# Performance work log

Measured on AMD Instinct MI355X. Metric: run time of the kernel, lower is better.

The kernel has to match this reference:

```python
import jax, jax.numpy as jnp
import numpy as np

N_EXPERTS = 8
TOP_K = 2
D_MODEL = 1024
N_TOKENS = 8192


def setup_inputs() -> dict:
    key = jax.random.key(0)
    k1, k2, k3, k4, k5 = jax.random.split(key, 5)
    x = jax.random.normal(k1, (N_TOKENS, D_MODEL), dtype=jnp.float32)
    # router Linear(num_experts): weight [d, E], bias [E]
    Wr = jax.random.normal(k2, (D_MODEL, N_EXPERTS), dtype=jnp.float32) / np.sqrt(D_MODEL)
    br = jnp.zeros((N_EXPERTS,), dtype=jnp.float32)
    # per-expert Linear(d_model): stacked weights [E, d, d], biases [E, d]
    W = jax.random.normal(k3, (N_EXPERTS, D_MODEL, D_MODEL), dtype=jnp.float32) / np.sqrt(D_MODEL)
    b = jnp.zeros((N_EXPERTS, D_MODEL), dtype=jnp.float32)
    return {"x": x, "Wr": Wr, "br": br, "W": W, "b": b}


def reference(x, Wr, br, W, b):
    # --- route ---
    logits = x @ Wr + br                                  # [N, E]
    top_k_vals, top_k_idxs = jax.lax.top_k(logits, TOP_K)  # [N, k]
    top_k_gates = jax.nn.softmax(top_k_vals, axis=-1)      # [N, k]
    # --- experts (dense form of gather-dispatch; same math as routed compute) ---
    y_all = jnp.einsum('nd,edh->neh', x, W) + b            # [N, E, d]
    # --- gather routed expert outputs per slot ---
    y_k = jnp.take_along_axis(y_all, top_k_idxs[:, :, None], axis=1)  # [N, k, d]
    # --- weighted scatter-combine (reduce) ---
    out = jnp.sum(top_k_gates[:, :, None] * y_k, axis=1)   # [N, d]
    return out
```

## Files before the change

### kernel.cpp

```cpp
#include <hip/hip_runtime.h>
#include <hip/hip_bf16.h>


#define NTOK 8192
#define DM   1024
#define NEXP 8
#define CAP  8192
#define MAXT 136

#define RBLK 1024
#define WBLK 512

typedef __attribute__((ext_vector_type(8))) short bf16x8;
typedef __attribute__((ext_vector_type(4))) float f32x4;

__device__ __forceinline__ unsigned short f2bf(float f) {
  unsigned u = __float_as_uint(f);
  unsigned r = (u + 0x7fffu + ((u >> 16) & 1u)) >> 16;
  return (unsigned short)r;
}
__device__ __forceinline__ float bf2f(unsigned short s) {
  return __uint_as_float(((unsigned)s) << 16);
}

__device__ __forceinline__ void gl_lds16(const void* g, void* l) {
  __builtin_amdgcn_global_load_lds(
      (const __attribute__((address_space(1))) unsigned int*)g,
      (__attribute__((address_space(3))) unsigned int*)l, 16, 0, 0);
}

__global__ __launch_bounds__(256) void router_kernel(
    const float* __restrict__ x, const float* __restrict__ Wr,
    const float* __restrict__ br, unsigned short* __restrict__ xbf,
    int4* __restrict__ topk, int* __restrict__ counts,
    int* __restrict__ tok, int2* __restrict__ pos,
    int* __restrict__ done, int* __restrict__ desc,
    int* __restrict__ ntiles, int* __restrict__ offset) {
  __shared__ int lcnt[NEXP];
  __shared__ int4 ltop[8];
  __shared__ int2 lrank[8];
  const int tid = threadIdx.x;
  const int rb = blockIdx.x;
  const int wave = tid >> 6, lane = tid & 63;
  const int tb = rb * 8 + wave * 2;
  if (tid < NEXP) lcnt[tid] = 0;

  const int l4 = lane * 4;

  float v[2][16];
#pragma unroll
  for (int tt = 0; tt < 2; tt++) {
#pragma unroll
    for (int i = 0; i < 4; i++) {
      float4 f = *(const float4*)(x + (size_t)(tb + tt) * DM + i * 256 + l4);
      v[tt][i * 4 + 0] = f.x; v[tt][i * 4 + 1] = f.y;
      v[tt][i * 4 + 2] = f.z; v[tt][i * 4 + 3] = f.w;
    }
  }
#pragma unroll
  for (int tt = 0; tt < 2; tt++) {
#pragma unroll
    for (int i = 0; i < 4; i++) {
      uint2 pk;
      pk.x = (unsigned)f2bf(v[tt][i * 4 + 0]) |
             ((unsigned)f2bf(v[tt][i * 4 + 1]) << 16);
      pk.y = (unsigned)f2bf(v[tt][i * 4 + 2]) |
             ((unsigned)f2bf(v[tt][i * 4 + 3]) << 16);
      *(uint2*)(xbf + (size_t)(tb + tt) * DM + i * 256 + l4) = pk;
    }
  }
  float p[2][8] = {};
#pragma unroll
  for (int i = 0; i < 4; i++) {
#pragma unroll
    for (int j = 0; j < 4; j++) {
      const float* wrow = Wr + (size_t)(i * 256 + l4 + j) * NEXP;
      float4 wl = *(const float4*)(wrow);
      float4 wh = *(const float4*)(wrow + 4);
#pragma unroll
      for (int tt = 0; tt < 2; tt++) {
        float xv = v[tt][i * 4 + j];
        p[tt][0] += xv * wl.x; p[tt][1] += xv * wl.y;
        p[tt][2] += xv * wl.z; p[tt][3] += xv * wl.w;
        p[tt][4] += xv * wh.x; p[tt][5] += xv * wh.y;
        p[tt][6] += xv * wh.z; p[tt][7] += xv * wh.w;
      }
    }
  }
#pragma unroll
  for (int off = 32; off >= 1; off >>= 1) {
#pragma unroll
    for (int tt = 0; tt < 2; tt++)
#pragma unroll
      for (int e = 0; e < 8; e++)
        p[tt][e] += __shfl_xor(p[tt][e], off, 64);
  }
  if (lane == 0) {
#pragma unroll
    for (int tt = 0; tt < 2; tt++) {
      float lg[8];
#pragma unroll
      for (int e = 0; e < 8; e++) lg[e] = p[tt][e] + br[e];
      float v0 = lg[0]; int i0 = 0;
#pragma unroll
      for (int e = 1; e < 8; e++) if (lg[e] > v0) { v0 = lg[e]; i0 = e; }
      float v1 = -3.4e38f; int i1 = 0;
#pragma unroll
      for (int e = 0; e < 8; e++)
        if (e != i0 && lg[e] > v1) { v1 = lg[e]; i1 = e; }
      float ee = __expf(v1 - v0);
      float g0 = 1.0f / (1.0f + ee);
      float g1 = ee / (1.0f + ee);
      int4 rec;
      rec.x = i0; rec.y = i1;
      rec.z = __float_as_int(g0); rec.w = __float_as_int(g1);
      ltop[wave * 2 + tt] = rec;
      topk[tb + tt] = rec;
    }
  }
  __syncthreads();

  if (tid < 8) {
    int4 r = ltop[tid];
    int s0 = atomicAdd(&lcnt[r.x], 1);
    int s1 = atomicAdd(&lcnt[r.y], 1);
    int2 rk; rk.x = s0; rk.y = s1;
    lrank[tid] = rk;
  }
  __syncthreads();
  if (tid < NEXP) lcnt[tid] = atomicAdd(&counts[tid], lcnt[tid]);
  __syncthreads();
  if (tid < 8) {
    int4 r = ltop[tid];
    int2 rk = lrank[tid];
    int p0 = lcnt[r.x] + rk.x;
    int p1 = lcnt[r.y] + rk.y;
    int t = rb * 8 + tid;
    tok[r.x * CAP + p0] = t;
    tok[r.y * CAP + p1] = t;
    int2 pr; pr.x = p0; pr.y = p1;
    pos[t] = pr;
  }
  __syncthreads();

  if (tid == 0) {
    __threadfence();
    if (atomicAdd(done, 1) == RBLK - 1) {
      __threadfence();
      int cnt[NEXP];
#pragma unroll
      for (int e = 0; e < NEXP; e++) cnt[e] = atomicAdd(&counts[e], 0);
      int idx = 0, off = 0;
#pragma unroll
      for (int e = 0; e < NEXP; e++) {
        offset[e] = off;
        off += cnt[e];
        int nm = (cnt[e] + 127) >> 7;
        for (int i = 0; i < nm; i++) desc[idx++] = (e << 16) | i;
      }
      *ntiles = idx;
    }
  }
}

__global__ __launch_bounds__(256) void wcast_kernel(
    const float* __restrict__ W, unsigned short* __restrict__ Wt) {
  __shared__ __align__(16) unsigned int smem[8192];
  const int tid = threadIdx.x;
  const int tb = blockIdx.x;
  const int e = tb >> 6;
  const int rem = tb & 63;
  const int D0 = (rem >> 3) * 128;
  const int H0 = (rem & 7) * 128;

  const int dp = tid >> 5;
  const int c  = tid & 31;
  const float* Wsrc = W + (size_t)e * DM * DM + (size_t)D0 * DM + H0 + c * 4;
#pragma unroll 4
  for (int i = 0; i < 8; i++) {
    const int dc = dp + 8 * i;
    const int d = dc * 2;
    float4 a = *(const float4*)(Wsrc + (size_t)d * DM);
    float4 b = *(const float4*)(Wsrc + (size_t)(d + 1) * DM);
    unsigned pk[4];
    pk[0] = (unsigned)f2bf(a.x) | ((unsigned)f2bf(b.x) << 16);
    pk[1] = (unsigned)f2bf(a.y) | ((unsigned)f2bf(b.y) << 16);
    pk[2] = (unsigned)f2bf(a.z) | ((unsigned)f2bf(b.z) << 16);
    pk[3] = (unsigned)f2bf(a.w) | ((unsigned)f2bf(b.w) << 16);
#pragma unroll
    for (int j = 0; j < 4; j++) {
      const int h = c * 4 + j;
      const int pg = ((dc >> 2) ^ (h >> 2)) & 15;
      smem[h * 64 + pg * 4 + (dc & 3)] = pk[j];
    }
  }
  __syncthreads();

  const int hh = tid >> 4;
  const int g  = tid & 15;
  unsigned short* Wdst = Wt + (size_t)e * DM * DM + (size_t)H0 * DM + D0;
#pragma unroll 4
  for (int o = 0; o < 8; o++) {
    const int h = hh + 16 * o;
    const int pg = (g ^ (h >> 2)) & 15;
    uint4 v = *(const uint4*)(smem + h * 64 + pg * 4);
    *(uint4*)(Wdst + (size_t)h * DM + g * 8) = v;
  }
}

__global__ __launch_bounds__(256) void moe_gemm_kernel(
    const unsigned short* __restrict__ xbf, const unsigned short* __restrict__ wt,
    const int* __restrict__ counts, const int* __restrict__ offset,
    const int* __restrict__ tok, const int* __restrict__ desc,
    const int* __restrict__ ntiles, unsigned short* __restrict__ ybuf) {
  const int slot = blockIdx.y;
  if (slot >= *ntiles) return;
  const int dsc = desc[slot];
  const int e = dsc >> 16;
  const int m0 = (dsc & 0xffff) * 128;
  const int cnt = counts[e];
  const int n0 = blockIdx.x * 128;

  __shared__ __align__(16) unsigned short sA0[128 * 32];
  __shared__ __align__(16) unsigned short sB0[128 * 32];
  __shared__ __align__(16) unsigned short sA1[128 * 32];
  __shared__ __align__(16) unsigned short sB1[128 * 32];
  __shared__ int sTok[128];

  const int tid = threadIdx.x, wave = tid >> 6, lane = tid & 63;

  if (tid < 128) {
    int sr = m0 + tid;
    int cl = (sr < cnt) ? sr : (cnt - 1);
    sTok[tid] = tok[e * CAP + cl];
  }
  __syncthreads();

  const int rA1 = wave * 16 + (lane >> 2);
  const int rA2 = rA1 + 64;
  const int cch = lane & 3;
  const int cg1 = (cch ^ ((rA1 >> 1) & 3)) * 8;
  const int cg2 = (cch ^ ((rA2 >> 1) & 3)) * 8;
  const unsigned short* pA1 = xbf + (size_t)sTok[rA1] * DM + cg1;
  const unsigned short* pA2 = xbf + (size_t)sTok[rA2] * DM + cg2;
  const unsigned short* wte = wt + (size_t)e * DM * DM;
  const unsigned short* pB1 = wte + (size_t)(n0 + rA1) * DM + cg1;
  const unsigned short* pB2 = wte + (size_t)(n0 + rA2) * DM + cg2;
  const int lo1 = wave * 512, lo2 = (wave + 4) * 512;

  const int q = lane >> 4, ml = lane & 15;
  const int wm = (wave >> 1) * 64, wn = (wave & 1) * 64;
  int offA[4], offB[4];
#pragma unroll
  for (int i = 0; i < 4; i++) {
    int row = wm + i * 16 + ml;
    offA[i] = row * 32 + (q ^ ((row >> 1) & 3)) * 8;
    int rowb = wn + i * 16 + ml;
    offB[i] = rowb * 32 + (q ^ ((rowb >> 1) & 3)) * 8;
  }

  f32x4 acc[4][4] = {};

  for (int k0 = 0; k0 < DM; k0 += 64) {
    gl_lds16(pA1 + k0, sA0 + lo1);
    gl_lds16(pA2 + k0, sA0 + lo2);
    gl_lds16(pB1 + k0, sB0 + lo1);
    gl_lds16(pB2 + k0, sB0 + lo2);
    gl_lds16(pA1 + k0 + 32, sA1 + lo1);
    gl_lds16(pA2 + k0 + 32, sA1 + lo2);
    gl_lds16(pB1 + k0 + 32, sB1 + lo1);
    gl_lds16(pB2 + k0 + 32, sB1 + lo2);
    __syncthreads();
    bf16x8 af0[4], bf0[4], af1[4], bf1[4];
#pragma unroll
    for (int i = 0; i < 4; i++) {
      af0[i] = *(const bf16x8*)(sA0 + offA[i]);
      bf0[i] = *(const bf16x8*)(sB0 + offB[i]);
      af1[i] = *(const bf16x8*)(sA1 + offA[i]);
      bf1[i] = *(const bf16x8*)(sB1 + offB[i]);
    }
#pragma unroll
    for (int mt = 0; mt < 4; mt++)
#pragma unroll
      for (int nt = 0; nt < 4; nt++)
        acc[mt][nt] = __builtin_amdgcn_mfma_f32_16x16x32_bf16(
            af0[mt], bf0[nt], acc[mt][nt], 0, 0, 0);
#pragma unroll
    for (int mt = 0; mt < 4; mt++)
#pragma unroll
      for (int nt = 0; nt < 4; nt++)
        acc[mt][nt] = __builtin_amdgcn_mfma_f32_16x16x32_bf16(
            af1[mt], bf1[nt], acc[mt][nt], 0, 0, 0);
    __syncthreads();
  }

  const int yb = offset[e] + m0;
#pragma unroll
  for (int mt = 0; mt < 4; mt++) {
    int rbase = wm + mt * 16 + q * 4;
#pragma unroll
    for (int r = 0; r < 4; r++) {
      int row = rbase + r;
      if (m0 + row >= cnt) continue;
      unsigned short* yrow = ybuf + (size_t)(yb + row) * DM + n0;
#pragma unroll
      for (int nt = 0; nt < 4; nt++) {
        yrow[wn + nt * 16 + ml] = f2bf(acc[mt][nt][r]);
      }
    }
  }
}

__global__ __launch_bounds__(256) void combine_kernel(
    const unsigned short* __restrict__ ybuf, const int4* __restrict__ topk,
    const int2* __restrict__ pos, const int* __restrict__ offset,
    const float* __restrict__ bias, float* __restrict__ out) {
  const int c = threadIdx.x * 4;
  const int t0 = blockIdx.x * 4;
#pragma unroll
  for (int i = 0; i < 4; i++) {
    const int t = t0 + i;
    int4 r = topk[t];
    int2 p = pos[t];
    float g0 = __int_as_float(r.z), g1 = __int_as_float(r.w);
    int s0 = offset[r.x] + p.x;
    int s1 = offset[r.y] + p.y;
    ushort4 ya = *(const ushort4*)(ybuf + (size_t)s0 * DM + c);
    ushort4 yb = *(const ushort4*)(ybuf + (size_t)s1 * DM + c);
    float4 b0 = *(const float4*)(bias + (size_t)r.x * DM + c);
    float4 b1 = *(const float4*)(bias + (size_t)r.y * DM + c);
    float4 o;
    o.x = g0 * (bf2f(ya.x) + b0.x) + g1 * (bf2f(yb.x) + b1.x);
    o.y = g0 * (bf2f(ya.y) + b0.y) + g1 * (bf2f(yb.y) + b1.y);
    o.z = g0 * (bf2f(ya.z) + b0.z) + g1 * (bf2f(yb.z) + b1.z);
    o.w = g0 * (bf2f(ya.w) + b0.w) + g1 * (bf2f(yb.w) + b1.w);
    *(float4*)(out + (size_t)t * DM + c) = o;
  }
}

extern "C" void kernel_launch(void* const* d_in, const int* in_sizes, int n_in,
                              void* d_out, int out_size, void* d_ws, size_t ws_size,
                              hipStream_t stream) {
  const float* x  = (const float*)d_in[0];
  const float* Wr = (const float*)d_in[1];
  const float* br = (const float*)d_in[2];
  const float* W  = (const float*)d_in[3];
  const float* b  = (const float*)d_in[4];
  float* out = (float*)d_out;

  char* ws = (char*)d_ws;
  unsigned short* xbf  = (unsigned short*)ws;
  unsigned short* wt   = (unsigned short*)(ws + (16u << 20));
  unsigned short* ybuf = (unsigned short*)(ws + (32u << 20));
  char* ctrl = ws + (64u << 20);
  int*   counts = (int*)ctrl;
  int*   ntiles = (int*)(ctrl + 64);
  int*   done   = (int*)(ctrl + 96);
  int*   offset = (int*)(ctrl + 128);
  int*   desc   = (int*)(ctrl + 256);
  int*   tok    = (int*)(ctrl + 4096);
  int2*  pos    = (int2*)(ctrl + 4096 + (256u << 10));
  int4*  topk   = (int4*)(ctrl + 4096 + (320u << 10));

  hipMemsetAsync(ctrl, 0, 128, stream);

  router_kernel<<<RBLK, 256, 0, stream>>>(
      x, Wr, br, xbf, topk, counts, tok, pos, done, desc, ntiles, offset);
  wcast_kernel<<<WBLK, 256, 0, stream>>>(W, wt);
  moe_gemm_kernel<<<dim3(8, MAXT), 256, 0, stream>>>(
      xbf, wt, counts, offset, tok, desc, ntiles, ybuf);
  combine_kernel<<<NTOK / 4, 256, 0, stream>>>(ybuf, topk, pos, offset, b, out);
}
```

Before: 225.7 us.

## Double-buffer MoE GEMM LDS tiles and remap block indices for weight reuse

Adds a second LDS buffer so the global-to-LDS loads for the next K step are issued before the MFMA work on the current step, overlapping memory latency with compute. It also remaps the linear block index so eight consecutive blocks cover different token tiles that share the same N column slice, which is meant to improve L2 reuse of expert weight columns. LDS use doubles to 64KB per block, which may reduce occupancy.

```diff
diff --git a/kernel.cpp b/kernel.cpp
--- a/kernel.cpp
+++ b/kernel.cpp
@@ -213,18 +213,17 @@
     const int* __restrict__ counts, const int* __restrict__ offset,
     const int* __restrict__ tok, const int* __restrict__ desc,
     const int* __restrict__ ntiles, unsigned short* __restrict__ ybuf) {
-  const int slot = blockIdx.y;
+  const int L = blockIdx.y * 8 + blockIdx.x;
+  const int slot = (L & 7) | ((L >> 6) << 3);
+  const int n0 = ((L >> 3) & 7) * 128;
   if (slot >= *ntiles) return;
   const int dsc = desc[slot];
   const int e = dsc >> 16;
   const int m0 = (dsc & 0xffff) * 128;
   const int cnt = counts[e];
-  const int n0 = blockIdx.x * 128;
-
-  __shared__ __align__(16) unsigned short sA0[128 * 32];
-  __shared__ __align__(16) unsigned short sB0[128 * 32];
-  __shared__ __align__(16) unsigned short sA1[128 * 32];
-  __shared__ __align__(16) unsigned short sB1[128 * 32];
+
+  __shared__ __align__(16) unsigned short sA[2][2][128 * 32];
+  __shared__ __align__(16) unsigned short sB[2][2][128 * 32];
   __shared__ int sTok[128];
 
   const int tid = threadIdx.x, wave = tid >> 6, lane = tid & 63;
@@ -259,25 +258,40 @@
     offB[i] = rowb * 32 + (q ^ ((rowb >> 1) & 3)) * 8;
   }
 
+#define STAGE(b, kk)                                  \
+  do {                                                \
+    gl_lds16(pA1 + (kk),      &sA[b][0][lo1]);        \
+    gl_lds16(pA2 + (kk),      &sA[b][0][lo2]);        \
+    gl_lds16(pB1 + (kk),      &sB[b][0][lo1]);        \
+    gl_lds16(pB2 + (kk),      &sB[b][0][lo2]);        \
+    gl_lds16(pA1 + (kk) + 32, &sA[b][1][lo1]);        \
+    gl_lds16(pA2 + (kk) + 32, &sA[b][1][lo2]);        \
+    gl_lds16(pB1 + (kk) + 32, &sB[b][1][lo1]);        \
+    gl_lds16(pB2 + (kk) + 32, &sB[b][1][lo2]);        \
+  } while (0)
+
   f32x4 acc[4][4] = {};
 
+  STAGE(0, 0);
+  asm volatile("s_waitcnt vmcnt(0)" ::: "memory");
+  __builtin_amdgcn_s_barrier();
+
+  int cur = 0;
   for (int k0 = 0; k0 < DM; k0 += 64) {
-    gl_lds16(pA1 + k0, sA0 + lo1);
-    gl_lds16(pA2 + k0, sA0 + lo2);
-    gl_lds16(pB1 + k0, sB0 + lo1);
-    gl_lds16(pB2 + k0, sB0 + lo2);
-    gl_lds16(pA1 + k0 + 32, sA1 + lo1);
-    gl_lds16(pA2 + k0 + 32, sA1 + lo2);
-    gl_lds16(pB1 + k0 + 32, sB1 + lo1);
-    gl_lds16(pB2 + k0 + 32, sB1 + lo2);
-    __syncthreads();
+    if (k0 + 64 < DM) STAGE(cur ^ 1, k0 + 64);
+    __builtin_amdgcn_sched_barrier(0);
+
+    const unsigned short* a0 = sA[cur][0];
+    const unsigned short* b0 = sB[cur][0];
+    const unsigned short* a1 = sA[cur][1];
+    const unsigned short* b1 = sB[cur][1];
     bf16x8 af0[4], bf0[4], af1[4], bf1[4];
 #pragma unroll
     for (int i = 0; i < 4; i++) {
-      af0[i] = *(const bf16x8*)(sA0 + offA[i]);
-      bf0[i] = *(const bf16x8*)(sB0 + offB[i]);
-      af1[i] = *(const bf16x8*)(sA1 + offA[i]);
-      bf1[i] = *(const bf16x8*)(sB1 + offB[i]);
+      af0[i] = *(const bf16x8*)(a0 + offA[i]);
+      bf0[i] = *(const bf16x8*)(b0 + offB[i]);
+      af1[i] = *(const bf16x8*)(a1 + offA[i]);
+      bf1[i] = *(const bf16x8*)(b1 + offB[i]);
     }
 #pragma unroll
     for (int mt = 0; mt < 4; mt++)
@@ -291,8 +305,12 @@
       for (int nt = 0; nt < 4; nt++)
         acc[mt][nt] = __builtin_amdgcn_mfma_f32_16x16x32_bf16(
             af1[mt], bf1[nt], acc[mt][nt], 0, 0, 0);
-    __syncthreads();
-  }
+
+    asm volatile("s_waitcnt vmcnt(0)" ::: "memory");
+    __builtin_amdgcn_s_barrier();
+    cur ^= 1;
+  }
+#undef STAGE
 
   const int yb = offset[e] + m0;
 #pragma unroll
```

Measured after the change: 231.5 us. 1.03x slower.

## Stage router weights in LDS, split tile building, remap GEMM block order

Applied to the files above, without the earlier changes.

The router kernel now copies Wr into padded shared memory and reads x with lane-strided scalar loads, replacing the per-lane float4 global loads of Wr. The last-block atomic counter that built the tile descriptors moves into a separate single-thread kernel, which removes the threadfence and done atomic. The GEMM block index is remapped so that 8 consecutive blocks cover 8 M-tiles for the same N column, aiming for better L2 reuse of expert weights. In exchange there is one extra kernel launch, a 36 KB LDS load in every router block, and narrower (scalar) global accesses.

```diff
diff --git a/kernel.cpp b/kernel.cpp
--- a/kernel.cpp
+++ b/kernel.cpp
@@ -33,58 +33,43 @@
     const float* __restrict__ x, const float* __restrict__ Wr,
     const float* __restrict__ br, unsigned short* __restrict__ xbf,
     int4* __restrict__ topk, int* __restrict__ counts,
-    int* __restrict__ tok, int2* __restrict__ pos,
-    int* __restrict__ done, int* __restrict__ desc,
-    int* __restrict__ ntiles, int* __restrict__ offset) {
-  __shared__ int lcnt[NEXP];
+    int* __restrict__ tok, int2* __restrict__ pos) {
+  __shared__ float sWr[1024 * 9];
+  __shared__ int  lcnt[NEXP];
   __shared__ int4 ltop[8];
   __shared__ int2 lrank[8];
   const int tid = threadIdx.x;
-  const int rb = blockIdx.x;
   const int wave = tid >> 6, lane = tid & 63;
-  const int tb = rb * 8 + wave * 2;
+  const int tb = blockIdx.x * 8 + wave * 2;
   if (tid < NEXP) lcnt[tid] = 0;
 
-  const int l4 = lane * 4;
-
-  float v[2][16];
+#pragma unroll
+  for (int it = 0; it < 4; it++) {
+    const int row = it * 256 + tid;
+    float4 w0 = *(const float4*)(Wr + (size_t)row * 8);
+    float4 w1 = *(const float4*)(Wr + (size_t)row * 8 + 4);
+    float* dst = &sWr[row * 9];
+    dst[0] = w0.x; dst[1] = w0.y; dst[2] = w0.z; dst[3] = w0.w;
+    dst[4] = w1.x; dst[5] = w1.y; dst[6] = w1.z; dst[7] = w1.w;
+  }
+  __syncthreads();
+
+  float p[2][8] = {{0}};
 #pragma unroll
   for (int tt = 0; tt < 2; tt++) {
-#pragma unroll
-    for (int i = 0; i < 4; i++) {
-      float4 f = *(const float4*)(x + (size_t)(tb + tt) * DM + i * 256 + l4);
-      v[tt][i * 4 + 0] = f.x; v[tt][i * 4 + 1] = f.y;
-      v[tt][i * 4 + 2] = f.z; v[tt][i * 4 + 3] = f.w;
-    }
-  }
-#pragma unroll
-  for (int tt = 0; tt < 2; tt++) {
-#pragma unroll
-    for (int i = 0; i < 4; i++) {
-      uint2 pk;
-      pk.x = (unsigned)f2bf(v[tt][i * 4 + 0]) |
-             ((unsigned)f2bf(v[tt][i * 4 + 1]) << 16);
-      pk.y = (unsigned)f2bf(v[tt][i * 4 + 2]) |
-             ((unsigned)f2bf(v[tt][i * 4 + 3]) << 16);
-      *(uint2*)(xbf + (size_t)(tb + tt) * DM + i * 256 + l4) = pk;
-    }
-  }
-  float p[2][8] = {};
-#pragma unroll
-  for (int i = 0; i < 4; i++) {
-#pragma unroll
-    for (int j = 0; j < 4; j++) {
-      const float* wrow = Wr + (size_t)(i * 256 + l4 + j) * NEXP;
-      float4 wl = *(const float4*)(wrow);
-      float4 wh = *(const float4*)(wrow + 4);
-#pragma unroll
-      for (int tt = 0; tt < 2; tt++) {
-        float xv = v[tt][i * 4 + j];
-        p[tt][0] += xv * wl.x; p[tt][1] += xv * wl.y;
-        p[tt][2] += xv * wl.z; p[tt][3] += xv * wl.w;
-        p[tt][4] += xv * wh.x; p[tt][5] += xv * wh.y;
-        p[tt][6] += xv * wh.z; p[tt][7] += xv * wh.w;
-      }
+    const float* xr = x + (size_t)(tb + tt) * DM + lane;
+    float v[16];
+#pragma unroll
+    for (int i = 0; i < 16; i++) v[i] = xr[i * 64];
+    unsigned short* xo = xbf + (size_t)(tb + tt) * DM + lane;
+#pragma unroll
+    for (int i = 0; i < 16; i++) xo[i * 64] = f2bf(v[i]);
+#pragma unroll
+    for (int i = 0; i < 16; i++) {
+      const float* wrow = &sWr[(i * 64 + lane) * 9];
+      float xv = v[i];
+#pragma unroll
+      for (int e = 0; e < 8; e++) p[tt][e] += xv * wrow[e];
     }
   }
 #pragma unroll
@@ -135,31 +120,27 @@
     int2 rk = lrank[tid];
     int p0 = lcnt[r.x] + rk.x;
     int p1 = lcnt[r.y] + rk.y;
-    int t = rb * 8 + tid;
+    int t = blockIdx.x * 8 + tid;
     tok[r.x * CAP + p0] = t;
     tok[r.y * CAP + p1] = t;
     int2 pr; pr.x = p0; pr.y = p1;
     pos[t] = pr;
   }
-  __syncthreads();
-
-  if (tid == 0) {
-    __threadfence();
-    if (atomicAdd(done, 1) == RBLK - 1) {
-      __threadfence();
-      int cnt[NEXP];
-#pragma unroll
-      for (int e = 0; e < NEXP; e++) cnt[e] = atomicAdd(&counts[e], 0);
-      int idx = 0, off = 0;
-#pragma unroll
-      for (int e = 0; e < NEXP; e++) {
-        offset[e] = off;
-        off += cnt[e];
-        int nm = (cnt[e] + 127) >> 7;
-        for (int i = 0; i < nm; i++) desc[idx++] = (e << 16) | i;
-      }
-      *ntiles = idx;
-    }
+}
+
+__global__ __launch_bounds__(64) void build_tiles_kernel(
+    const int* __restrict__ counts, int* __restrict__ desc,
+    int* __restrict__ ntiles, int* __restrict__ offset) {
+  if (threadIdx.x == 0) {
+    int idx = 0, off = 0;
+#pragma unroll
+    for (int e = 0; e < NEXP; e++) {
+      offset[e] = off;
+      off += counts[e];
+      int nm = (counts[e] + 127) >> 7;
+      for (int i = 0; i < nm; i++) desc[idx++] = (e << 16) | i;
+    }
+    *ntiles = idx;
   }
 }
 
@@ -213,13 +194,14 @@
     const int* __restrict__ counts, const int* __restrict__ offset,
     const int* __restrict__ tok, const int* __restrict__ desc,
     const int* __restrict__ ntiles, unsigned short* __restrict__ ybuf) {
-  const int slot = blockIdx.y;
+  const int L = blockIdx.y * 8 + blockIdx.x;
+  const int slot = (L & 7) | ((L >> 6) << 3);
+  const int n0 = ((L >> 3) & 7) * 128;
   if (slot >= *ntiles) return;
   const int dsc = desc[slot];
   const int e = dsc >> 16;
   const int m0 = (dsc & 0xffff) * 128;
   const int cnt = counts[e];
-  const int n0 = blockIdx.x * 128;
 
   __shared__ __align__(16) unsigned short sA0[128 * 32];
   __shared__ __align__(16) unsigned short sB0[128 * 32];
@@ -355,7 +337,6 @@
   char* ctrl = ws + (64u << 20);
   int*   counts = (int*)ctrl;
   int*   ntiles = (int*)(ctrl + 64);
-  int*   done   = (int*)(ctrl + 96);
   int*   offset = (int*)(ctrl + 128);
   int*   desc   = (int*)(ctrl + 256);
   int*   tok    = (int*)(ctrl + 4096);
@@ -365,8 +346,9 @@
   hipMemsetAsync(ctrl, 0, 128, stream);
 
   router_kernel<<<RBLK, 256, 0, stream>>>(
-      x, Wr, br, xbf, topk, counts, tok, pos, done, desc, ntiles, offset);
+      x, Wr, br, xbf, topk, counts, tok, pos);
   wcast_kernel<<<WBLK, 256, 0, stream>>>(W, wt);
+  build_tiles_kernel<<<1, 64, 0, stream>>>(counts, desc, ntiles, offset);
   moe_gemm_kernel<<<dim3(8, MAXT), 256, 0, stream>>>(
       xbf, wt, counts, offset, tok, desc, ntiles, ybuf);
   combine_kernel<<<NTOK / 4, 256, 0, stream>>>(ybuf, topk, pos, offset, b, out);
```

After: 196.2 us. -13.1%, faster.
